# Performance work log

Hardware: AMD Instinct MI355X
Metric: run time of the kernel (lower is better)

## Reference

```python
import jax, jax.numpy as jnp
import numpy as np


def _conv1x1(x, w, b):
    # x: (B,C,H,W), w: (O,C), b: (O,)
    return jnp.einsum('bchw,oc->bohw', x, w) + b[None, :, None, None]


def setup_inputs() -> dict:
    key = jax.random.key(0)
    ks = jax.random.split(key, 10)
    B, C, H, W = 8, 64, 64, 64
    x = jax.random.normal(ks[0], (B, C, H, W), dtype=jnp.float32)
    s = 0.05
    params = {}
    names = ['wq', 'wQ', 'wK', 'wV']
    for i, n in enumerate(names):
        params[n] = jax.random.normal(ks[1 + 2 * i], (C, C), dtype=jnp.float32) * s
        params['b' + n[1:]] = jax.random.normal(ks[2 + 2 * i], (C,), dtype=jnp.float32) * s
    return dict(x=x, wq=params['wq'], bq=params['bq'], wQ=params['wQ'], bQ=params['bQ'],
                wK=params['wK'], bK=params['bK'], wV=params['wV'], bV=params['bV'],
                gamma=jnp.ones((1,), dtype=jnp.float32))


def reference(x, wq, bq, wQ, bQ, wK, bK, wV, bV, gamma):
    B, C, H, W = x.shape
    # q = query_conv(x).view(B,-1,W,H)  (pure reshape, matches torch .view on contiguous tensor)
    q = _conv1x1(x, wq, bq).reshape(B, C, W, H)
    # 2x2 average pool, stride 2
    qp = q.reshape(B, C, W // 2, 2, H // 2, 2).mean(axis=(3, 5))
    q_ = qp.reshape(B, C, (W * H) // 4)          # (B, C, N/4)
    K = _conv1x1(x, wK, bK).reshape(B, C, H * W)  # (B, C, N)
    V = _conv1x1(x, wV, bV).reshape(B, C, H * W)  # (B, C, N)
    # stage 1: pooled queries attend over all keys
    attn1 = jax.nn.softmax(jnp.einsum('bcp,bcn->bpn', q_, K), axis=-1)  # (B, N/4, N)
    out = jnp.einsum('bcn,bpn->bcp', V, attn1)                           # (B, C, N/4)
    # stage 2: full queries attend over pooled anchors
    Q = _conv1x1(x, wQ, bQ).reshape(B, C, H * W)                         # (B, C, N)
    attn2 = jax.nn.softmax(jnp.einsum('bcn,bcp->bnp', Q, q_), axis=-1)   # (B, N, N/4)
    out = jnp.einsum('bcp,bnp->bcn', out, attn2)                         # (B, C, N)
    out = out.reshape(B, C, H, W)
    return gamma * out + x
```

## Files before the change

### kernel.cpp

```cpp
#include <hip/hip_runtime.h>
#include <hip/hip_bf16.h>


typedef float  f32x4  __attribute__((ext_vector_type(4)));
typedef __bf16 bf16x8 __attribute__((ext_vector_type(8)));
typedef __bf16 bf16x4 __attribute__((ext_vector_type(4)));

__device__ __forceinline__ int swz(int ch) { return ch ^ ((ch >> 3) & 7); }

__global__ __launch_bounds__(256) void conv4_kernel(
    const float* __restrict__ x,
    const float* __restrict__ wq, const float* __restrict__ bq,
    const float* __restrict__ wQ, const float* __restrict__ bQ,
    const float* __restrict__ wK, const float* __restrict__ bK,
    const float* __restrict__ wV, const float* __restrict__ bV,
    __bf16* __restrict__ Kt, __bf16* __restrict__ Vc,
    __bf16* __restrict__ Qt, __bf16* __restrict__ qt)
{
  __shared__ float xs[64 * 132];
  __shared__ float wsh[64 * 68];

  const int tid = threadIdx.x;
  const int m   = blockIdx.x >> 8;
  const int b   = (blockIdx.x >> 5) & 7;
  const int rp  = blockIdx.x & 31;
  const int n0  = rp << 7;

  const float* wg = (m == 0) ? wK : (m == 1) ? wV : (m == 2) ? wQ : wq;
  const float* bg = (m == 0) ? bK : (m == 1) ? bV : (m == 2) ? bQ : bq;

  for (int i = tid; i < 64 * 32; i += 256) {
    int c = i >> 5, j = i & 31;
    *(f32x4*)&xs[c * 132 + j * 4] =
        *(const f32x4*)&x[((size_t)(b * 64 + c)) * 4096 + n0 + j * 4];
  }
  for (int i = tid; i < 1024; i += 256) {
    int o = i >> 4, c0 = (i & 15) << 2;
    f32x4 v = *(const f32x4*)&wg[o * 64 + c0];
    wsh[(c0 + 0) * 68 + o] = v[0];
    wsh[(c0 + 1) * 68 + o] = v[1];
    wsh[(c0 + 2) * 68 + o] = v[2];
    wsh[(c0 + 3) * 68 + o] = v[3];
  }
  __syncthreads();

  const int ty = tid >> 4, tx = tid & 15;

  float acc[4][8];
  {
    f32x4 bv = *(const f32x4*)&bg[ty * 4];
#pragma unroll
    for (int i = 0; i < 4; ++i)
#pragma unroll
      for (int j = 0; j < 8; ++j) acc[i][j] = bv[i];
  }

#pragma unroll 4
  for (int c = 0; c < 64; ++c) {
    f32x4 wv = *(const f32x4*)&wsh[c * 68 + ty * 4];
    f32x4 xa = *(const f32x4*)&xs[c * 132 + tx * 8];
    f32x4 xb = *(const f32x4*)&xs[c * 132 + tx * 8 + 4];
#pragma unroll
    for (int i = 0; i < 4; ++i) {
#pragma unroll
      for (int j = 0; j < 4; ++j) {
        acc[i][j]     += wv[i] * xa[j];
        acc[i][j + 4] += wv[i] * xb[j];
      }
    }
  }

  if (m == 0 || m == 2) {
    __bf16* dst = (m == 0) ? Kt : Qt;
#pragma unroll
    for (int j = 0; j < 8; ++j) {
      int n = n0 + tx * 8 + j;
      bf16x4 pk;
#pragma unroll
      for (int i = 0; i < 4; ++i) pk[i] = (__bf16)acc[i][j];
      *(bf16x4*)&dst[((size_t)(b * 4096 + n)) * 64 + ty * 4] = pk;
    }
  } else if (m == 1) {
#pragma unroll
    for (int i = 0; i < 4; ++i) {
      int o = ty * 4 + i;
      bf16x8 pk;
#pragma unroll
      for (int j = 0; j < 8; ++j) pk[j] = (__bf16)acc[i][j];
      *(bf16x8*)&Vc[((size_t)(b * 64 + o)) * 4096 + n0 + tx * 8] = pk;
    }
  } else {
    float pl[4][4];
#pragma unroll
    for (int i = 0; i < 4; ++i)
#pragma unroll
      for (int jj = 0; jj < 4; ++jj)
        pl[i][jj] = acc[i][2 * jj] + acc[i][2 * jj + 1];
#pragma unroll
    for (int i = 0; i < 4; ++i)
#pragma unroll
      for (int jj = 0; jj < 4; ++jj)
        pl[i][jj] += __shfl_xor(pl[i][jj], 8);
    if (tx < 8) {
#pragma unroll
      for (int jj = 0; jj < 4; ++jj) {
        int p = rp * 32 + tx * 4 + jj;
        bf16x4 pk;
#pragma unroll
        for (int i = 0; i < 4; ++i) pk[i] = (__bf16)(0.25f * pl[i][jj]);
        *(bf16x4*)&qt[((size_t)(b * 1024 + p)) * 64 + ty * 4] = pk;
      }
    }
  }
}

__global__ __launch_bounds__(512, 2) void attn1_kernel(
    const __bf16* __restrict__ Qg,
    const __bf16* __restrict__ Kg,
    const __bf16* __restrict__ Vg,
    __bf16* __restrict__ outp)
{
  __shared__ __align__(16) char smem[147456];

  const int tid  = threadIdx.x;
  const int wave = tid >> 6, lane = tid & 63;
  const int lg = (lane >> 4) & 3, lp = lane & 15;
  const int qt = wave & 1, ks = wave >> 1;
  const int b  = blockIdx.x >> 5;
  const int q0 = (blockIdx.x & 31) * 32;

  const __bf16* qg = Qg + ((size_t)(b * 1024 + q0 + qt * 16 + lp)) * 64;
  const bf16x8 qf0 = *(const bf16x8*)(qg + lg * 8);
  const bf16x8 qf1 = *(const bf16x8*)(qg + 32 + lg * 8);

  f32x4 acc[4];
#pragma unroll
  for (int ct = 0; ct < 4; ++ct) acc[ct] = (f32x4){0.f, 0.f, 0.f, 0.f};
  float m_run = -3.0e38f, l_run = 0.0f;

  bf16x8 kreg[4], vreg[4];
  const int sw = swz(tid & 511);
  auto load_tile = [&](int r) {
    const __bf16* kb = Kg + (size_t)b * 262144 + (size_t)r * 4096 + tid * 8;
    const __bf16* vb = Vg + ((size_t)(b * 64 + (tid >> 3))) * 4096 + r * 64 + (tid & 7) * 8;
#pragma unroll
    for (int j = 0; j < 4; ++j) {
      kreg[j] = *(const bf16x8*)(kb + (size_t)j * 65536);
      vreg[j] = *(const bf16x8*)(vb + j * 1024);
    }
  };
  auto write_tile = [&](int nb) {
    __bf16* kd = (__bf16*)(smem + nb * 32768);
    __bf16* vd = (__bf16*)(smem + 65536 + nb * 32768);
#pragma unroll
    for (int j = 0; j < 4; ++j) {
      *(bf16x8*)(kd + (j * 512 + sw) * 8) = kreg[j];
      *(bf16x8*)(vd + (j * 512 + sw) * 8) = vreg[j];
    }
  };

  load_tile(0); write_tile(0);
  load_tile(1);
  __syncthreads();

  for (int r = 0; r < 16; ++r) {
    const int cur = r & 1;
    if (r + 1 < 16) write_tile(cur ^ 1);
    if (r + 2 < 16) load_tile(r + 2);

    const __bf16* lK = (const __bf16*)(smem + cur * 32768) + ks * 4096;
    const __bf16* lV = (const __bf16*)(smem + 65536 + cur * 32768) + ks * 4096;
    __bf16* lP = (__bf16*)(smem + 131072) + wave * 1024;

    f32x4 S[4];
#pragma unroll
    for (int mt = 0; mt < 4; ++mt) {
      int ch0 = (mt * 16 + lp) * 8 + lg;
      bf16x8 a0 = *(const bf16x8*)(lK + swz(ch0) * 8);
      bf16x8 a1 = *(const bf16x8*)(lK + swz(ch0 + 4) * 8);
      f32x4 z = (f32x4){0.f, 0.f, 0.f, 0.f};
      z = __builtin_amdgcn_mfma_f32_16x16x32_bf16(a0, qf0, z, 0, 0, 0);
      z = __builtin_amdgcn_mfma_f32_16x16x32_bf16(a1, qf1, z, 0, 0, 0);
      S[mt] = z;
    }

    float tmax = -3.0e38f;
#pragma unroll
    for (int mt = 0; mt < 4; ++mt)
#pragma unroll
      for (int rr = 0; rr < 4; ++rr) tmax = fmaxf(tmax, S[mt][rr]);
    tmax = fmaxf(tmax, __shfl_xor(tmax, 16));
    tmax = fmaxf(tmax, __shfl_xor(tmax, 32));
    float mnew = fmaxf(m_run, tmax);
    float sc = __expf(m_run - mnew);
    float rs = 0.f;
#pragma unroll
    for (int mt = 0; mt < 4; ++mt)
#pragma unroll
      for (int rr = 0; rr < 4; ++rr) {
        float e = __expf(S[mt][rr] - mnew);
        S[mt][rr] = e;
        rs += e;
      }
    rs += __shfl_xor(rs, 16);
    rs += __shfl_xor(rs, 32);
    l_run = l_run * sc + rs;
    m_run = mnew;
#pragma unroll
    for (int ct = 0; ct < 4; ++ct) acc[ct] *= sc;

#pragma unroll
    for (int mt = 0; mt < 4; ++mt) {
      bf16x4 pk;
#pragma unroll
      for (int rr = 0; rr < 4; ++rr) pk[rr] = (__bf16)S[mt][rr];
      int boff = lp * 128 + mt * 32 + lg * 8;
      *(bf16x4*)((char*)lP + (boff ^ ((lp & 7) << 4))) = pk;
    }

    {
      int chp = lp * 8 + lg;
      bf16x8 pf0 = *(const bf16x8*)(lP + swz(chp) * 8);
      bf16x8 pf1 = *(const bf16x8*)(lP + swz(chp + 4) * 8);
#pragma unroll
      for (int ct = 0; ct < 4; ++ct) {
        int chv = (ct * 16 + lp) * 8 + lg;
        bf16x8 v0 = *(const bf16x8*)(lV + swz(chv) * 8);
        bf16x8 v1 = *(const bf16x8*)(lV + swz(chv + 4) * 8);
        acc[ct] = __builtin_amdgcn_mfma_f32_16x16x32_bf16(v0, pf0, acc[ct], 0, 0, 0);
        acc[ct] = __builtin_amdgcn_mfma_f32_16x16x32_bf16(v1, pf1, acc[ct], 0, 0, 0);
      }
    }
    __syncthreads();
  }

  float2* mlb = (float2*)(smem + 131072);
  if (lg == 0) mlb[wave * 16 + lp] = make_float2(m_run, l_run);
  float* cb = (float*)smem;
  {
    float* myc = cb + ((size_t)(qt * 4 + ks) * 16 + lp) * 64;
#pragma unroll
    for (int ct = 0; ct < 4; ++ct)
      *(f32x4*)(myc + ct * 16 + lg * 4) = acc[ct];
  }
  __syncthreads();

  if (wave < 2) {
    const int qtt = wave;
    const int nq = q0 + qtt * 16 + lp;
    float mm[4], lv[4];
    float mstar = -3.0e38f;
#pragma unroll
    for (int s = 0; s < 4; ++s) {
      float2 v = mlb[(s * 2 + qtt) * 16 + lp];
      mm[s] = v.x; lv[s] = v.y;
      mstar = fmaxf(mstar, mm[s]);
    }
    float f[4], lstar = 0.f;
#pragma unroll
    for (int s = 0; s < 4; ++s) {
      f[s] = __expf(mm[s] - mstar);
      lstar += lv[s] * f[s];
    }
    float inv = 1.0f / lstar;
#pragma unroll
    for (int ct = 0; ct < 4; ++ct) {
      f32x4 o = (f32x4){0.f, 0.f, 0.f, 0.f};
#pragma unroll
      for (int s = 0; s < 4; ++s) {
        f32x4 t = *(const f32x4*)(cb + ((size_t)(qtt * 4 + s) * 16 + lp) * 64 +
                                  ct * 16 + lg * 4);
        o += f[s] * t;
      }
#pragma unroll
      for (int rr = 0; rr < 4; ++rr) {
        int c = ct * 16 + lg * 4 + rr;
        outp[((size_t)(b * 64 + c)) * 1024 + nq] = (__bf16)(o[rr] * inv);
      }
    }
  }
}

__global__ __launch_bounds__(512, 2) void attn2_kernel(
    const __bf16* __restrict__ Qg,
    const __bf16* __restrict__ Kg,
    const __bf16* __restrict__ Vg,
    float* __restrict__ outp,
    const float* __restrict__ xres,
    const float* __restrict__ gammap)
{
  __shared__ __align__(16) char smem[49152];

  const int tid  = threadIdx.x;
  const int wave = tid >> 6, lane = tid & 63;
  const int lg = (lane >> 4) & 3, lp = lane & 15;
  const int b  = blockIdx.x >> 5;
  const int q0 = (blockIdx.x & 31) * 128;
  const int myq = q0 + wave * 16 + lp;

  const __bf16* qg = Qg + ((size_t)(b * 4096 + myq)) * 64;
  const bf16x8 qf0 = *(const bf16x8*)(qg + lg * 8);
  const bf16x8 qf1 = *(const bf16x8*)(qg + 32 + lg * 8);

  f32x4 acc[4];
#pragma unroll
  for (int ct = 0; ct < 4; ++ct) acc[ct] = (f32x4){0.f, 0.f, 0.f, 0.f};
  float m_run = -3.0e38f, l_run = 0.0f;

  bf16x8 kreg, vreg;
  const int sw = swz(tid & 511);
  auto load_tile = [&](int r) {
    kreg = *(const bf16x8*)(Kg + (size_t)b * 65536 + (size_t)r * 4096 + tid * 8);
    vreg = *(const bf16x8*)(Vg + ((size_t)(b * 64 + (tid >> 3))) * 1024 + r * 64 + (tid & 7) * 8);
  };
  auto write_tile = [&](int nb) {
    *(bf16x8*)((__bf16*)(smem + nb * 8192) + sw * 8) = kreg;
    *(bf16x8*)((__bf16*)(smem + 16384 + nb * 8192) + sw * 8) = vreg;
  };

  load_tile(0); write_tile(0);
  load_tile(1);
  __syncthreads();

  for (int r = 0; r < 16; ++r) {
    const int cur = r & 1;
    if (r + 1 < 16) write_tile(cur ^ 1);
    if (r + 2 < 16) load_tile(r + 2);

    const __bf16* lK = (const __bf16*)(smem + cur * 8192);
    const __bf16* lV = (const __bf16*)(smem + 16384 + cur * 8192);
    __bf16* lP = (__bf16*)(smem + 32768) + wave * 1024;

    f32x4 S[4];
#pragma unroll
    for (int mt = 0; mt < 4; ++mt) {
      int ch0 = (mt * 16 + lp) * 8 + lg;
      bf16x8 a0 = *(const bf16x8*)(lK + swz(ch0) * 8);
      bf16x8 a1 = *(const bf16x8*)(lK + swz(ch0 + 4) * 8);
      f32x4 z = (f32x4){0.f, 0.f, 0.f, 0.f};
      z = __builtin_amdgcn_mfma_f32_16x16x32_bf16(a0, qf0, z, 0, 0, 0);
      z = __builtin_amdgcn_mfma_f32_16x16x32_bf16(a1, qf1, z, 0, 0, 0);
      S[mt] = z;
    }

    float tmax = -3.0e38f;
#pragma unroll
    for (int mt = 0; mt < 4; ++mt)
#pragma unroll
      for (int rr = 0; rr < 4; ++rr) tmax = fmaxf(tmax, S[mt][rr]);
    tmax = fmaxf(tmax, __shfl_xor(tmax, 16));
    tmax = fmaxf(tmax, __shfl_xor(tmax, 32));
    float mnew = fmaxf(m_run, tmax);
    float sc = __expf(m_run - mnew);
    float rs = 0.f;
#pragma unroll
    for (int mt = 0; mt < 4; ++mt)
#pragma unroll
      for (int rr = 0; rr < 4; ++rr) {
        float e = __expf(S[mt][rr] - mnew);
        S[mt][rr] = e;
        rs += e;
      }
    rs += __shfl_xor(rs, 16);
    rs += __shfl_xor(rs, 32);
    l_run = l_run * sc + rs;
    m_run = mnew;
#pragma unroll
    for (int ct = 0; ct < 4; ++ct) acc[ct] *= sc;

#pragma unroll
    for (int mt = 0; mt < 4; ++mt) {
      bf16x4 pk;
#pragma unroll
      for (int rr = 0; rr < 4; ++rr) pk[rr] = (__bf16)S[mt][rr];
      int boff = lp * 128 + mt * 32 + lg * 8;
      *(bf16x4*)((char*)lP + (boff ^ ((lp & 7) << 4))) = pk;
    }

    {
      int chp = lp * 8 + lg;
      bf16x8 pf0 = *(const bf16x8*)(lP + swz(chp) * 8);
      bf16x8 pf1 = *(const bf16x8*)(lP + swz(chp + 4) * 8);
#pragma unroll
      for (int ct = 0; ct < 4; ++ct) {
        int chv = (ct * 16 + lp) * 8 + lg;
        bf16x8 v0 = *(const bf16x8*)(lV + swz(chv) * 8);
        bf16x8 v1 = *(const bf16x8*)(lV + swz(chv + 4) * 8);
        acc[ct] = __builtin_amdgcn_mfma_f32_16x16x32_bf16(v0, pf0, acc[ct], 0, 0, 0);
        acc[ct] = __builtin_amdgcn_mfma_f32_16x16x32_bf16(v1, pf1, acc[ct], 0, 0, 0);
      }
    }
    __syncthreads();
  }

  const float inv = 1.0f / l_run;
  const float g0 = gammap[0];
#pragma unroll
  for (int ct = 0; ct < 4; ++ct)
#pragma unroll
    for (int rr = 0; rr < 4; ++rr) {
      int c = ct * 16 + lg * 4 + rr;
      size_t oi = ((size_t)(b * 64 + c)) * 4096 + myq;
      outp[oi] = g0 * (acc[ct][rr] * inv) + xres[oi];
    }
}

extern "C" void kernel_launch(void* const* d_in, const int* in_sizes, int n_in,
                              void* d_out, int out_size, void* d_ws, size_t ws_size,
                              hipStream_t stream) {
  const float* x     = (const float*)d_in[0];
  const float* wq    = (const float*)d_in[1];
  const float* bq    = (const float*)d_in[2];
  const float* wQ    = (const float*)d_in[3];
  const float* bQ    = (const float*)d_in[4];
  const float* wK    = (const float*)d_in[5];
  const float* bK    = (const float*)d_in[6];
  const float* wV    = (const float*)d_in[7];
  const float* bV    = (const float*)d_in[8];
  const float* gamma = (const float*)d_in[9];

  __bf16* ws = (__bf16*)d_ws;
  __bf16* Kt = ws;
  __bf16* Vc = ws + 2097152;
  __bf16* Qt = ws + 4194304;
  __bf16* qt = ws + 6291456;
  __bf16* O1 = ws + 6815744;

  hipLaunchKernelGGL(conv4_kernel, dim3(1024), dim3(256), 0, stream,
                     x, wq, bq, wQ, bQ, wK, bK, wV, bV, Kt, Vc, Qt, qt);
  hipLaunchKernelGGL(attn1_kernel, dim3(256), dim3(512), 0, stream,
                     qt, Kt, Vc, O1);
  hipLaunchKernelGGL(attn2_kernel, dim3(256), dim3(512), 0, stream,
                     Qt, qt, O1, (float*)d_out, x, gamma);
}
```

Baseline: 75.64 us.

## Split-K attention stage one across blocks with combine kernel; split attn2 keys intra-block

Attention stage one now splits the key dimension across 8 blocks per query tile. Each block writes unnormalized partial outputs and running max/sum to workspace, and a new combine kernel merges them. This doubles the grid and cuts shared memory so more blocks fit per CU. Attention stage two now splits keys across two wave groups inside a block with an in-block merge, doubling its grid. The conv kernel moves to 128 threads with an 8x8 register tile per thread. The trade-off is an extra launch plus float32 partial-result traffic through global memory.

```diff
diff --git a/kernel.cpp b/kernel.cpp
--- a/kernel.cpp
+++ b/kernel.cpp
@@ -8,7 +8,7 @@
 
 __device__ __forceinline__ int swz(int ch) { return ch ^ ((ch >> 3) & 7); }
 
-__global__ __launch_bounds__(256) void conv4_kernel(
+__global__ __launch_bounds__(128) void conv4_kernel(
     const float* __restrict__ x,
     const float* __restrict__ wq, const float* __restrict__ bq,
     const float* __restrict__ wQ, const float* __restrict__ bQ,
@@ -29,12 +29,12 @@
   const float* wg = (m == 0) ? wK : (m == 1) ? wV : (m == 2) ? wQ : wq;
   const float* bg = (m == 0) ? bK : (m == 1) ? bV : (m == 2) ? bQ : bq;
 
-  for (int i = tid; i < 64 * 32; i += 256) {
+  for (int i = tid; i < 64 * 32; i += 128) {
     int c = i >> 5, j = i & 31;
     *(f32x4*)&xs[c * 132 + j * 4] =
         *(const f32x4*)&x[((size_t)(b * 64 + c)) * 4096 + n0 + j * 4];
   }
-  for (int i = tid; i < 1024; i += 256) {
+  for (int i = tid; i < 1024; i += 128) {
     int o = i >> 4, c0 = (i & 15) << 2;
     f32x4 v = *(const f32x4*)&wg[o * 64 + c0];
     wsh[(c0 + 0) * 68 + o] = v[0];
@@ -46,26 +46,31 @@
 
   const int ty = tid >> 4, tx = tid & 15;
 
-  float acc[4][8];
+  float acc[8][8];
   {
-    f32x4 bv = *(const f32x4*)&bg[ty * 4];
-#pragma unroll
-    for (int i = 0; i < 4; ++i)
-#pragma unroll
-      for (int j = 0; j < 8; ++j) acc[i][j] = bv[i];
+    f32x4 bv0 = *(const f32x4*)&bg[ty * 8];
+    f32x4 bv1 = *(const f32x4*)&bg[ty * 8 + 4];
+#pragma unroll
+    for (int j = 0; j < 8; ++j) {
+#pragma unroll
+      for (int i = 0; i < 4; ++i) { acc[i][j] = bv0[i]; acc[i + 4][j] = bv1[i]; }
+    }
   }
 
 #pragma unroll 4
   for (int c = 0; c < 64; ++c) {
-    f32x4 wv = *(const f32x4*)&wsh[c * 68 + ty * 4];
-    f32x4 xa = *(const f32x4*)&xs[c * 132 + tx * 8];
-    f32x4 xb = *(const f32x4*)&xs[c * 132 + tx * 8 + 4];
+    f32x4 wv0 = *(const f32x4*)&wsh[c * 68 + ty * 8];
+    f32x4 wv1 = *(const f32x4*)&wsh[c * 68 + ty * 8 + 4];
+    f32x4 xa  = *(const f32x4*)&xs[c * 132 + tx * 8];
+    f32x4 xb  = *(const f32x4*)&xs[c * 132 + tx * 8 + 4];
 #pragma unroll
     for (int i = 0; i < 4; ++i) {
 #pragma unroll
       for (int j = 0; j < 4; ++j) {
-        acc[i][j]     += wv[i] * xa[j];
-        acc[i][j + 4] += wv[i] * xb[j];
+        acc[i][j]         += wv0[i] * xa[j];
+        acc[i][j + 4]     += wv0[i] * xb[j];
+        acc[i + 4][j]     += wv1[i] * xa[j];
+        acc[i + 4][j + 4] += wv1[i] * xb[j];
       }
     }
   }
@@ -75,29 +80,29 @@
 #pragma unroll
     for (int j = 0; j < 8; ++j) {
       int n = n0 + tx * 8 + j;
-      bf16x4 pk;
-#pragma unroll
-      for (int i = 0; i < 4; ++i) pk[i] = (__bf16)acc[i][j];
-      *(bf16x4*)&dst[((size_t)(b * 4096 + n)) * 64 + ty * 4] = pk;
+      bf16x8 pk;
+#pragma unroll
+      for (int i = 0; i < 8; ++i) pk[i] = (__bf16)acc[i][j];
+      *(bf16x8*)&dst[((size_t)(b * 4096 + n)) * 64 + ty * 8] = pk;
     }
   } else if (m == 1) {
 #pragma unroll
-    for (int i = 0; i < 4; ++i) {
-      int o = ty * 4 + i;
+    for (int i = 0; i < 8; ++i) {
+      int o = ty * 8 + i;
       bf16x8 pk;
 #pragma unroll
       for (int j = 0; j < 8; ++j) pk[j] = (__bf16)acc[i][j];
       *(bf16x8*)&Vc[((size_t)(b * 64 + o)) * 4096 + n0 + tx * 8] = pk;
     }
   } else {
-    float pl[4][4];
-#pragma unroll
-    for (int i = 0; i < 4; ++i)
+    float pl[8][4];
+#pragma unroll
+    for (int i = 0; i < 8; ++i)
 #pragma unroll
       for (int jj = 0; jj < 4; ++jj)
         pl[i][jj] = acc[i][2 * jj] + acc[i][2 * jj + 1];
 #pragma unroll
-    for (int i = 0; i < 4; ++i)
+    for (int i = 0; i < 8; ++i)
 #pragma unroll
       for (int jj = 0; jj < 4; ++jj)
         pl[i][jj] += __shfl_xor(pl[i][jj], 8);
@@ -105,31 +110,33 @@
 #pragma unroll
       for (int jj = 0; jj < 4; ++jj) {
         int p = rp * 32 + tx * 4 + jj;
-        bf16x4 pk;
-#pragma unroll
-        for (int i = 0; i < 4; ++i) pk[i] = (__bf16)(0.25f * pl[i][jj]);
-        *(bf16x4*)&qt[((size_t)(b * 1024 + p)) * 64 + ty * 4] = pk;
+        bf16x8 pk;
+#pragma unroll
+        for (int i = 0; i < 8; ++i) pk[i] = (__bf16)(0.25f * pl[i][jj]);
+        *(bf16x8*)&qt[((size_t)(b * 1024 + p)) * 64 + ty * 8] = pk;
       }
     }
   }
 }
 
-__global__ __launch_bounds__(512, 2) void attn1_kernel(
+__global__ __launch_bounds__(512, 4) void attn1_kernel(
     const __bf16* __restrict__ Qg,
     const __bf16* __restrict__ Kg,
     const __bf16* __restrict__ Vg,
-    __bf16* __restrict__ outp)
+    float* __restrict__ partO,
+    float2* __restrict__ partML)
 {
-  __shared__ __align__(16) char smem[147456];
+  __shared__ __align__(16) char smem[49152];
 
   const int tid  = threadIdx.x;
   const int wave = tid >> 6, lane = tid & 63;
   const int lg = (lane >> 4) & 3, lp = lane & 15;
-  const int qt = wave & 1, ks = wave >> 1;
-  const int b  = blockIdx.x >> 5;
-  const int q0 = (blockIdx.x & 31) * 32;
-
-  const __bf16* qg = Qg + ((size_t)(b * 1024 + q0 + qt * 16 + lp)) * 64;
+  const int b  = blockIdx.x >> 6;
+  const int qb = (blockIdx.x >> 3) & 7;
+  const int ks = blockIdx.x & 7;
+
+  const int qw = wave * 16 + lp;
+  const __bf16* qg = Qg + ((size_t)(b * 1024 + qb * 128 + qw)) * 64;
   const bf16x8 qf0 = *(const bf16x8*)(qg + lg * 8);
   const bf16x8 qf1 = *(const bf16x8*)(qg + 32 + lg * 8);
 
@@ -138,39 +145,30 @@
   for (int ct = 0; ct < 4; ++ct) acc[ct] = (f32x4){0.f, 0.f, 0.f, 0.f};
   float m_run = -3.0e38f, l_run = 0.0f;
 
-  bf16x8 kreg[4], vreg[4];
+  bf16x8 kreg, vreg;
   const int sw = swz(tid & 511);
   auto load_tile = [&](int r) {
-    const __bf16* kb = Kg + (size_t)b * 262144 + (size_t)r * 4096 + tid * 8;
-    const __bf16* vb = Vg + ((size_t)(b * 64 + (tid >> 3))) * 4096 + r * 64 + (tid & 7) * 8;
-#pragma unroll
-    for (int j = 0; j < 4; ++j) {
-      kreg[j] = *(const bf16x8*)(kb + (size_t)j * 65536);
-      vreg[j] = *(const bf16x8*)(vb + j * 1024);
-    }
+    int kv0 = ks * 512 + r * 64;
+    kreg = *(const bf16x8*)(Kg + ((size_t)(b * 4096 + kv0 + (tid >> 3))) * 64 + (tid & 7) * 8);
+    vreg = *(const bf16x8*)(Vg + ((size_t)(b * 64 + (tid >> 3))) * 4096 + kv0 + (tid & 7) * 8);
   };
   auto write_tile = [&](int nb) {
-    __bf16* kd = (__bf16*)(smem + nb * 32768);
-    __bf16* vd = (__bf16*)(smem + 65536 + nb * 32768);
-#pragma unroll
-    for (int j = 0; j < 4; ++j) {
-      *(bf16x8*)(kd + (j * 512 + sw) * 8) = kreg[j];
-      *(bf16x8*)(vd + (j * 512 + sw) * 8) = vreg[j];
-    }
+    *(bf16x8*)((__bf16*)(smem + nb * 8192) + sw * 8) = kreg;
+    *(bf16x8*)((__bf16*)(smem + 16384 + nb * 8192) + sw * 8) = vreg;
   };
 
   load_tile(0); write_tile(0);
   load_tile(1);
   __syncthreads();
 
-  for (int r = 0; r < 16; ++r) {
+  for (int r = 0; r < 8; ++r) {
     const int cur = r & 1;
-    if (r + 1 < 16) write_tile(cur ^ 1);
-    if (r + 2 < 16) load_tile(r + 2);
-
-    const __bf16* lK = (const __bf16*)(smem + cur * 32768) + ks * 4096;
-    const __bf16* lV = (const __bf16*)(smem + 65536 + cur * 32768) + ks * 4096;
-    __bf16* lP = (__bf16*)(smem + 131072) + wave * 1024;
+    if (r + 1 < 8) write_tile(cur ^ 1);
+    if (r + 2 < 8) load_tile(r + 2);
+
+    const __bf16* lK = (const __bf16*)(smem + cur * 8192);
+    const __bf16* lV = (const __bf16*)(smem + 16384 + cur * 8192);
+    __bf16* lP = (__bf16*)(smem + 32768) + wave * 1024;
 
     f32x4 S[4];
 #pragma unroll
@@ -234,54 +232,60 @@
     __syncthreads();
   }
 
-  float2* mlb = (float2*)(smem + 131072);
-  if (lg == 0) mlb[wave * 16 + lp] = make_float2(m_run, l_run);
-  float* cb = (float*)smem;
-  {
-    float* myc = cb + ((size_t)(qt * 4 + ks) * 16 + lp) * 64;
-#pragma unroll
-    for (int ct = 0; ct < 4; ++ct)
-      *(f32x4*)(myc + ct * 16 + lg * 4) = acc[ct];
-  }
-  __syncthreads();
-
-  if (wave < 2) {
-    const int qtt = wave;
-    const int nq = q0 + qtt * 16 + lp;
-    float mm[4], lv[4];
+  const size_t pbase = ((size_t)(b * 8 + qb)) * 8 + ks;
+  if (lg == 0) partML[pbase * 128 + qw] = make_float2(m_run, l_run);
+  float* po = partO + pbase * 64 * 128;
+#pragma unroll
+  for (int ct = 0; ct < 4; ++ct)
+#pragma unroll
+    for (int rr = 0; rr < 4; ++rr)
+      po[(ct * 16 + lg * 4 + rr) * 128 + qw] = acc[ct][rr];
+}
+
+__global__ __launch_bounds__(256) void combine1_kernel(
+    const float* __restrict__ partO, const float2* __restrict__ partML,
+    __bf16* __restrict__ O1)
+{
+  __shared__ float fs[8][128];
+  __shared__ float inv[128];
+
+  const int tid = threadIdx.x;
+  const int b   = blockIdx.x >> 5;
+  const int qb  = (blockIdx.x >> 2) & 7;
+  const int c0  = (blockIdx.x & 3) * 16;
+  const size_t mbase = ((size_t)(b * 8 + qb)) * 8;
+
+  if (tid < 128) {
+    float mm[8], lv[8];
     float mstar = -3.0e38f;
 #pragma unroll
-    for (int s = 0; s < 4; ++s) {
-      float2 v = mlb[(s * 2 + qtt) * 16 + lp];
+    for (int s = 0; s < 8; ++s) {
+      float2 v = partML[(mbase + s) * 128 + tid];
       mm[s] = v.x; lv[s] = v.y;
       mstar = fmaxf(mstar, mm[s]);
     }
-    float f[4], lstar = 0.f;
-#pragma unroll
-    for (int s = 0; s < 4; ++s) {
-      f[s] = __expf(mm[s] - mstar);
-      lstar += lv[s] * f[s];
-    }
-    float inv = 1.0f / lstar;
-#pragma unroll
-    for (int ct = 0; ct < 4; ++ct) {
-      f32x4 o = (f32x4){0.f, 0.f, 0.f, 0.f};
-#pragma unroll
-      for (int s = 0; s < 4; ++s) {
-        f32x4 t = *(const f32x4*)(cb + ((size_t)(qtt * 4 + s) * 16 + lp) * 64 +
-                                  ct * 16 + lg * 4);
-        o += f[s] * t;
-      }
-#pragma unroll
-      for (int rr = 0; rr < 4; ++rr) {
-        int c = ct * 16 + lg * 4 + rr;
-        outp[((size_t)(b * 64 + c)) * 1024 + nq] = (__bf16)(o[rr] * inv);
-      }
-    }
+    float l = 0.f;
+#pragma unroll
+    for (int s = 0; s < 8; ++s) {
+      float fv = __expf(mm[s] - mstar);
+      fs[s][tid] = fv;
+      l += lv[s] * fv;
+    }
+    inv[tid] = 1.0f / l;
+  }
+  __syncthreads();
+
+  for (int i = tid; i < 2048; i += 256) {
+    int cl = i >> 7, q = i & 127, c = c0 + cl;
+    float o = 0.f;
+#pragma unroll
+    for (int s = 0; s < 8; ++s)
+      o += fs[s][q] * partO[((mbase + s) * 64 + c) * 128 + q];
+    O1[((size_t)(b * 64 + c)) * 1024 + qb * 128 + q] = (__bf16)(o * inv[q]);
   }
 }
 
-__global__ __launch_bounds__(512, 2) void attn2_kernel(
+__global__ __launch_bounds__(512, 4) void attn2_kernel(
     const __bf16* __restrict__ Qg,
     const __bf16* __restrict__ Kg,
     const __bf16* __restrict__ Vg,
@@ -289,14 +293,15 @@
     const float* __restrict__ xres,
     const float* __restrict__ gammap)
 {
-  __shared__ __align__(16) char smem[49152];
+  __shared__ __align__(16) char smem[81920];
 
   const int tid  = threadIdx.x;
   const int wave = tid >> 6, lane = tid & 63;
   const int lg = (lane >> 4) & 3, lp = lane & 15;
-  const int b  = blockIdx.x >> 5;
-  const int q0 = (blockIdx.x & 31) * 128;
-  const int myq = q0 + wave * 16 + lp;
+  const int qt4 = wave & 3, ks = wave >> 2;
+  const int b  = blockIdx.x >> 6;
+  const int q0 = (blockIdx.x & 63) * 64;
+  const int myq = q0 + qt4 * 16 + lp;
 
   const __bf16* qg = Qg + ((size_t)(b * 4096 + myq)) * 64;
   const bf16x8 qf0 = *(const bf16x8*)(qg + lg * 8);
@@ -307,29 +312,41 @@
   for (int ct = 0; ct < 4; ++ct) acc[ct] = (f32x4){0.f, 0.f, 0.f, 0.f};
   float m_run = -3.0e38f, l_run = 0.0f;
 
-  bf16x8 kreg, vreg;
-  const int sw = swz(tid & 511);
+  bf16x8 kreg[2], vreg[2];
+  const int cs = tid & 255;
+  const int sp = tid >> 8;
+  const int sw0 = swz(cs), sw1 = swz(cs + 256);
   auto load_tile = [&](int r) {
-    kreg = *(const bf16x8*)(Kg + (size_t)b * 65536 + (size_t)r * 4096 + tid * 8);
-    vreg = *(const bf16x8*)(Vg + ((size_t)(b * 64 + (tid >> 3))) * 1024 + r * 64 + (tid & 7) * 8);
+    int a0 = sp * 512 + r * 64;
+#pragma unroll
+    for (int j = 0; j < 2; ++j) {
+      int s = cs + j * 256;
+      int row = s >> 3, col = (s & 7) * 8;
+      kreg[j] = *(const bf16x8*)(Kg + ((size_t)(b * 1024 + a0 + row)) * 64 + col);
+      vreg[j] = *(const bf16x8*)(Vg + ((size_t)(b * 64 + row)) * 1024 + a0 + col);
+    }
   };
   auto write_tile = [&](int nb) {
-    *(bf16x8*)((__bf16*)(smem + nb * 8192) + sw * 8) = kreg;
-    *(bf16x8*)((__bf16*)(smem + 16384 + nb * 8192) + sw * 8) = vreg;
+    __bf16* kd = (__bf16*)(smem + (sp * 2 + nb) * 8192);
+    __bf16* vd = (__bf16*)(smem + 32768 + (sp * 2 + nb) * 8192);
+    *(bf16x8*)(kd + sw0 * 8) = kreg[0];
+    *(bf16x8*)(kd + sw1 * 8) = kreg[1];
+    *(bf16x8*)(vd + sw0 * 8) = vreg[0];
+    *(bf16x8*)(vd + sw1 * 8) = vreg[1];
   };
 
   load_tile(0); write_tile(0);
   load_tile(1);
   __syncthreads();
 
-  for (int r = 0; r < 16; ++r) {
+  for (int r = 0; r < 8; ++r) {
     const int cur = r & 1;
-    if (r + 1 < 16) write_tile(cur ^ 1);
-    if (r + 2 < 16) load_tile(r + 2);
-
-    const __bf16* lK = (const __bf16*)(smem + cur * 8192);
-    const __bf16* lV = (const __bf16*)(smem + 16384 + cur * 8192);
-    __bf16* lP = (__bf16*)(smem + 32768) + wave * 1024;
+    if (r + 1 < 8) write_tile(cur ^ 1);
+    if (r + 2 < 8) load_tile(r + 2);
+
+    const __bf16* lK = (const __bf16*)(smem + (ks * 2 + cur) * 8192);
+    const __bf16* lV = (const __bf16*)(smem + 32768 + (ks * 2 + cur) * 8192);
+    __bf16* lP = (__bf16*)(smem + 65536) + wave * 1024;
 
     f32x4 S[4];
 #pragma unroll
@@ -393,16 +410,41 @@
     __syncthreads();
   }
 
-  const float inv = 1.0f / l_run;
-  const float g0 = gammap[0];
-#pragma unroll
-  for (int ct = 0; ct < 4; ++ct)
-#pragma unroll
-    for (int rr = 0; rr < 4; ++rr) {
-      int c = ct * 16 + lg * 4 + rr;
-      size_t oi = ((size_t)(b * 64 + c)) * 4096 + myq;
-      outp[oi] = g0 * (acc[ct][rr] * inv) + xres[oi];
-    }
+  float2* mlb = (float2*)(smem + 65536);
+  if (lg == 0) mlb[wave * 16 + lp] = make_float2(m_run, l_run);
+  float* cb = (float*)smem;
+  {
+    float* myc = cb + ((size_t)((qt4 * 2 + ks) * 16 + lp)) * 64;
+#pragma unroll
+    for (int ct = 0; ct < 4; ++ct)
+      *(f32x4*)(myc + ct * 16 + lg * 4) = acc[ct];
+  }
+  __syncthreads();
+
+  if (wave < 4) {
+    const int qtt = wave;
+    const int nq = q0 + qtt * 16 + lp;
+    float2 v0 = mlb[qtt * 16 + lp];
+    float2 v1 = mlb[(qtt + 4) * 16 + lp];
+    float mstar = fmaxf(v0.x, v1.x);
+    float f0 = __expf(v0.x - mstar), f1 = __expf(v1.x - mstar);
+    float inv = 1.0f / (v0.y * f0 + v1.y * f1);
+    float g0 = gammap[0];
+#pragma unroll
+    for (int ct = 0; ct < 4; ++ct) {
+      f32x4 t0 = *(const f32x4*)(cb + ((size_t)((qtt * 2 + 0) * 16 + lp)) * 64 +
+                                 ct * 16 + lg * 4);
+      f32x4 t1 = *(const f32x4*)(cb + ((size_t)((qtt * 2 + 1) * 16 + lp)) * 64 +
+                                 ct * 16 + lg * 4);
+      f32x4 o = f0 * t0 + f1 * t1;
+#pragma unroll
+      for (int rr = 0; rr < 4; ++rr) {
+        int c = ct * 16 + lg * 4 + rr;
+        size_t oi = ((size_t)(b * 64 + c)) * 4096 + nq;
+        outp[oi] = g0 * (o[rr] * inv) + xres[oi];
+      }
+    }
+  }
 }
 
 extern "C" void kernel_launch(void* const* d_in, const int* in_sizes, int n_in,
@@ -425,11 +467,15 @@
   __bf16* Qt = ws + 4194304;
   __bf16* qt = ws + 6291456;
   __bf16* O1 = ws + 6815744;
-
-  hipLaunchKernelGGL(conv4_kernel, dim3(1024), dim3(256), 0, stream,
+  float*  partO  = (float*)((char*)d_ws + (16u << 20));
+  float2* partML = (float2*)((char*)d_ws + (32u << 20));
+
+  hipLaunchKernelGGL(conv4_kernel, dim3(1024), dim3(128), 0, stream,
                      x, wq, bq, wQ, bQ, wK, bK, wV, bV, Kt, Vc, Qt, qt);
-  hipLaunchKernelGGL(attn1_kernel, dim3(256), dim3(512), 0, stream,
-                     qt, Kt, Vc, O1);
-  hipLaunchKernelGGL(attn2_kernel, dim3(256), dim3(512), 0, stream,
+  hipLaunchKernelGGL(attn1_kernel, dim3(512), dim3(512), 0, stream,
+                     qt, Kt, Vc, partO, partML);
+  hipLaunchKernelGGL(combine1_kernel, dim3(256), dim3(256), 0, stream,
+                     partO, partML, O1);
+  hipLaunchKernelGGL(attn2_kernel, dim3(512), dim3(512), 0, stream,
                      Qt, qt, O1, (float*)d_out, x, gamma);
 }
```

New measurement: 81.06 us. +7.2%, slower.
